# Kernel optimization log

Hardware: AMD Instinct MI355X
Metric: run time of the kernel (lower is better)

## Reference

```python
import jax, jax.numpy as jnp
import numpy as np

T = 0.1          # temperature from CLloss.__init__
PD_EPS = 1e-6    # nn.PairwiseDistance default eps (added to the difference)
NORM_EPS = 1e-12 # F.normalize eps


def setup_inputs() -> dict:
    key = jax.random.key(0)
    k1, k2 = jax.random.split(key)
    embed = jax.random.normal(k1, (16384, 2048), dtype=jnp.float32)
    labels = jax.random.randint(k2, (16384, 20), 0, 2, dtype=jnp.int32)
    return {"embed": embed, "labels": labels}


def reference(embed, labels):
    lab = labels.astype(jnp.float32)
    n = embed.shape[0]
    # F.normalize(embed, dim=-1): x / max(||x||, eps)
    norm = jnp.maximum(jnp.linalg.norm(embed, axis=-1, keepdims=True), NORM_EPS)
    e = embed / norm
    # NOTE: original torch code has `return loss` inside the outer loop, so only
    # anchor i=0 contributes. Faithfully reproduce that.
    # pairwise distance: ||e0 - ej + eps||_2 for j = 1..n-1
    d = jnp.linalg.norm(e[0] - e[1:] + PD_EPS, axis=-1)            # [n-1]
    log_sim = -d / T                                               # log exp(-d/t)
    c = jnp.dot(lab[1:], lab[0])                                   # [n-1] label overlap counts
    Ci = 1e-12 + jnp.sum(c)
    Ei = 1e-12 + jnp.sum(jnp.exp(log_sim))
    # Li = sum_j -(c_j/Ci) * log(exp(-d_j/t)/Ei)
    Li = jnp.sum(-(c / Ci) * (log_sim - jnp.log(Ei)))
    return Li / n
```

## Files before the change

kernel.cpp:

```cpp
#include <hip/hip_runtime.h>
#include <math.h>

#define NROW 16384
#define DIM 2048
#define NLAB 20
#define T_INV 10.0f
#define PD_EPS 1e-6f
#define NORM_EPS 1e-12f

#define MAIN_BLOCKS 1024
#define THREADS 256
#define WS_PARTIALS_OFS 2560

__global__ __launch_bounds__(THREADS) void prep_kernel(const float* __restrict__ embed,
                                                       float* __restrict__ ws) {
    __shared__ float red[THREADS / 64];
    const int tid = threadIdx.x;
    const int lane = tid & 63, wid = tid >> 6;

    const float4* row0 = (const float4*)embed;
    float s = 0.f;
    for (int i = tid; i < DIM / 4; i += THREADS) {
        float4 v = row0[i];
        s += v.x * v.x + v.y * v.y + v.z * v.z + v.w * v.w;
    }
    for (int o = 32; o; o >>= 1) s += __shfl_xor(s, o, 64);
    if (lane == 0) red[wid] = s;
    __syncthreads();
    float tot = red[0] + red[1] + red[2] + red[3];
    float inv = 1.0f / fmaxf(sqrtf(tot), NORM_EPS);

    float saa = 0.f;
    float4* a4 = (float4*)ws;
    for (int i = tid; i < DIM / 4; i += THREADS) {
        float4 v = row0[i];
        float4 w;
        w.x = v.x * inv + PD_EPS;
        w.y = v.y * inv + PD_EPS;
        w.z = v.z * inv + PD_EPS;
        w.w = v.w * inv + PD_EPS;
        a4[i] = w;
        saa += w.x * w.x + w.y * w.y + w.z * w.z + w.w * w.w;
    }
    for (int o = 32; o; o >>= 1) saa += __shfl_xor(saa, o, 64);
    __syncthreads();
    if (lane == 0) red[wid] = saa;
    __syncthreads();
    if (tid == 0) ws[DIM] = red[0] + red[1] + red[2] + red[3];
}

__global__ __launch_bounds__(THREADS) void main_kernel(const float* __restrict__ embed,
                                                       const int* __restrict__ labels,
                                                       const float* __restrict__ ws) {
    __shared__ float a_lds[DIM];
    __shared__ float wsum[THREADS / 64][3];

    const int tid = threadIdx.x;
    const int lane = tid & 63, wid = tid >> 6;

    {
        const float4* src = (const float4*)ws;
        float4* dst = (float4*)a_lds;
        for (int i = tid; i < DIM / 4; i += THREADS) dst[i] = src[i];
    }
    const float S_aa = ws[DIM];
    __syncthreads();

    const float lab0 = (lane < NLAB) ? (float)labels[lane] : 0.f;

    const int gw = blockIdx.x * (THREADS / 64) + wid;
    const int nwaves = gridDim.x * (THREADS / 64);

    float acc_e = 0.f, acc_c = 0.f, acc_cl = 0.f;

    for (int row = 1 + gw; row < NROW; row += nwaves) {
        const float4* b4 = (const float4*)(embed + (size_t)row * DIM);
        const float4* a4 = (const float4*)a_lds;
        float sab = 0.f, sbb = 0.f;
#pragma unroll
        for (int it = 0; it < DIM / 4 / 64; ++it) {
            float4 bv = b4[it * 64 + lane];
            float4 av = a4[it * 64 + lane];
            sab += av.x * bv.x + av.y * bv.y + av.z * bv.z + av.w * bv.w;
            sbb += bv.x * bv.x + bv.y * bv.y + bv.z * bv.z + bv.w * bv.w;
        }
        float c = (lane < NLAB) ? lab0 * (float)labels[row * NLAB + lane] : 0.f;

        for (int o = 32; o; o >>= 1) {
            sab += __shfl_xor(sab, o, 64);
            sbb += __shfl_xor(sbb, o, 64);
            c   += __shfl_xor(c,   o, 64);
        }
        float inv = 1.0f / fmaxf(sqrtf(sbb), NORM_EPS);
        float d2 = S_aa + inv * (inv * sbb - 2.0f * sab);
        d2 = fmaxf(d2, 0.f);
        float ls = -sqrtf(d2) * T_INV;
        acc_e += expf(ls);
        acc_c += c;
        acc_cl += c * ls;
    }

    if (lane == 0) {
        wsum[wid][0] = acc_e;
        wsum[wid][1] = acc_c;
        wsum[wid][2] = acc_cl;
    }
    __syncthreads();
    if (tid == 0) {
        float se = 0.f, sc = 0.f, scl = 0.f;
        for (int w = 0; w < THREADS / 64; ++w) {
            se += wsum[w][0];
            sc += wsum[w][1];
            scl += wsum[w][2];
        }
        float* p = (float*)wsum;
        (void)p;
        float* partials = (float*)0;
        (void)partials;
        ((float*)ws)[0] = ((float*)ws)[0];
        float* wsw = const_cast<float*>(ws);
        wsw[WS_PARTIALS_OFS + blockIdx.x * 3 + 0] = se;
        wsw[WS_PARTIALS_OFS + blockIdx.x * 3 + 1] = sc;
        wsw[WS_PARTIALS_OFS + blockIdx.x * 3 + 2] = scl;
    }
}

__global__ __launch_bounds__(THREADS) void final_kernel(const float* __restrict__ ws,
                                                        float* __restrict__ out) {
    __shared__ float red[THREADS / 64][3];
    const int tid = threadIdx.x;
    const int lane = tid & 63, wid = tid >> 6;

    float se = 0.f, sc = 0.f, scl = 0.f;
    for (int i = tid; i < MAIN_BLOCKS; i += THREADS) {
        se  += ws[WS_PARTIALS_OFS + i * 3 + 0];
        sc  += ws[WS_PARTIALS_OFS + i * 3 + 1];
        scl += ws[WS_PARTIALS_OFS + i * 3 + 2];
    }
    for (int o = 32; o; o >>= 1) {
        se  += __shfl_xor(se,  o, 64);
        sc  += __shfl_xor(sc,  o, 64);
        scl += __shfl_xor(scl, o, 64);
    }
    if (lane == 0) { red[wid][0] = se; red[wid][1] = sc; red[wid][2] = scl; }
    __syncthreads();
    if (tid == 0) {
        se = sc = scl = 0.f;
        for (int w = 0; w < THREADS / 64; ++w) {
            se += red[w][0]; sc += red[w][1]; scl += red[w][2];
        }
        float Ci = 1e-12f + sc;
        float Ei = 1e-12f + se;
        float Li = (sc * logf(Ei) - scl) / Ci;
        out[0] = Li / (float)NROW;
    }
}

extern "C" void kernel_launch(void* const* d_in, const int* in_sizes, int n_in,
                              void* d_out, int out_size, void* d_ws, size_t ws_size,
                              hipStream_t stream) {
    const float* embed = (const float*)d_in[0];
    const int* labels = (const int*)d_in[1];
    float* out = (float*)d_out;
    float* ws = (float*)d_ws;

    prep_kernel<<<1, THREADS, 0, stream>>>(embed, ws);
    main_kernel<<<MAIN_BLOCKS, THREADS, 0, stream>>>(embed, labels, ws);
    final_kernel<<<1, THREADS, 0, stream>>>(ws, out);
}
```

Before: 196.5 us.

## Fuse prep, main and final kernels into one kernel with atomic last-block reduction

Merges the three kernels into one. Each wave recomputes the normalized anchor row 0 into registers instead of staging it through workspace and LDS. Cross-block reduction now uses float atomics plus a completion counter, with the last block computing the loss. The grid doubles to 2048 blocks. This removes two launches and the serialized single-block prep and final phases, at the cost of a redundant row-0 read per wave, more registers, a memset, and nondeterministic float summation order.

```diff
diff --git a/kernel.cpp b/kernel.cpp
--- a/kernel.cpp
+++ b/kernel.cpp
@@ -8,81 +8,60 @@
 #define PD_EPS 1e-6f
 #define NORM_EPS 1e-12f
 
-#define MAIN_BLOCKS 1024
+#define BLOCKS 2048
 #define THREADS 256
-#define WS_PARTIALS_OFS 2560
+#define WPB (THREADS / 64)
+#define TOTAL_WAVES (BLOCKS * WPB)
+#define FRAG 8
 
-__global__ __launch_bounds__(THREADS) void prep_kernel(const float* __restrict__ embed,
-                                                       float* __restrict__ ws) {
-    __shared__ float red[THREADS / 64];
+
+__global__ __launch_bounds__(THREADS) void clloss_kernel(const float* __restrict__ embed,
+                                                         const int* __restrict__ labels,
+                                                         float* __restrict__ ws,
+                                                         float* __restrict__ out) {
     const int tid = threadIdx.x;
-    const int lane = tid & 63, wid = tid >> 6;
+    const int lane = tid & 63;
+    const int wid = tid >> 6;
 
     const float4* row0 = (const float4*)embed;
+    float4 v[FRAG];
+#pragma unroll
+    for (int it = 0; it < FRAG; ++it) v[it] = row0[it * 64 + lane];
+
     float s = 0.f;
-    for (int i = tid; i < DIM / 4; i += THREADS) {
-        float4 v = row0[i];
-        s += v.x * v.x + v.y * v.y + v.z * v.z + v.w * v.w;
-    }
+#pragma unroll
+    for (int it = 0; it < FRAG; ++it)
+        s += v[it].x * v[it].x + v[it].y * v[it].y + v[it].z * v[it].z + v[it].w * v[it].w;
     for (int o = 32; o; o >>= 1) s += __shfl_xor(s, o, 64);
-    if (lane == 0) red[wid] = s;
-    __syncthreads();
-    float tot = red[0] + red[1] + red[2] + red[3];
-    float inv = 1.0f / fmaxf(sqrtf(tot), NORM_EPS);
+    const float inv0 = 1.0f / fmaxf(sqrtf(s), NORM_EPS);
 
+    float4 av[FRAG];
     float saa = 0.f;
-    float4* a4 = (float4*)ws;
-    for (int i = tid; i < DIM / 4; i += THREADS) {
-        float4 v = row0[i];
-        float4 w;
-        w.x = v.x * inv + PD_EPS;
-        w.y = v.y * inv + PD_EPS;
-        w.z = v.z * inv + PD_EPS;
-        w.w = v.w * inv + PD_EPS;
-        a4[i] = w;
-        saa += w.x * w.x + w.y * w.y + w.z * w.z + w.w * w.w;
+#pragma unroll
+    for (int it = 0; it < FRAG; ++it) {
+        av[it].x = v[it].x * inv0 + PD_EPS;
+        av[it].y = v[it].y * inv0 + PD_EPS;
+        av[it].z = v[it].z * inv0 + PD_EPS;
+        av[it].w = v[it].w * inv0 + PD_EPS;
+        saa += av[it].x * av[it].x + av[it].y * av[it].y +
+               av[it].z * av[it].z + av[it].w * av[it].w;
     }
     for (int o = 32; o; o >>= 1) saa += __shfl_xor(saa, o, 64);
-    __syncthreads();
-    if (lane == 0) red[wid] = saa;
-    __syncthreads();
-    if (tid == 0) ws[DIM] = red[0] + red[1] + red[2] + red[3];
-}
-
-__global__ __launch_bounds__(THREADS) void main_kernel(const float* __restrict__ embed,
-                                                       const int* __restrict__ labels,
-                                                       const float* __restrict__ ws) {
-    __shared__ float a_lds[DIM];
-    __shared__ float wsum[THREADS / 64][3];
-
-    const int tid = threadIdx.x;
-    const int lane = tid & 63, wid = tid >> 6;
-
-    {
-        const float4* src = (const float4*)ws;
-        float4* dst = (float4*)a_lds;
-        for (int i = tid; i < DIM / 4; i += THREADS) dst[i] = src[i];
-    }
-    const float S_aa = ws[DIM];
-    __syncthreads();
+    const float S_aa = saa;
 
     const float lab0 = (lane < NLAB) ? (float)labels[lane] : 0.f;
 
-    const int gw = blockIdx.x * (THREADS / 64) + wid;
-    const int nwaves = gridDim.x * (THREADS / 64);
-
+    const int gw = blockIdx.x * WPB + wid;
     float acc_e = 0.f, acc_c = 0.f, acc_cl = 0.f;
 
-    for (int row = 1 + gw; row < NROW; row += nwaves) {
+    for (int row = 1 + gw; row < NROW; row += TOTAL_WAVES) {
         const float4* b4 = (const float4*)(embed + (size_t)row * DIM);
-        const float4* a4 = (const float4*)a_lds;
         float sab = 0.f, sbb = 0.f;
 #pragma unroll
-        for (int it = 0; it < DIM / 4 / 64; ++it) {
-            float4 bv = b4[it * 64 + lane];
-            float4 av = a4[it * 64 + lane];
-            sab += av.x * bv.x + av.y * bv.y + av.z * bv.z + av.w * bv.w;
-            sbb += bv.x * bv.x + bv.y * bv.y + bv.z * bv.z + bv.w * bv.w;
+        for (int it = 0; it < FRAG; ++it) {
+            float4 b = b4[it * 64 + lane];
+            sab += av[it].x * b.x + av[it].y * b.y + av[it].z * b.z + av[it].w * b.w;
+            sbb += b.x * b.x + b.y * b.y + b.z * b.z + b.w * b.w;
         }
         float c = (lane < NLAB) ? lab0 * (float)labels[row * NLAB + lane] : 0.f;
 
@@ -91,15 +70,15 @@
             sbb += __shfl_xor(sbb, o, 64);
             c   += __shfl_xor(c,   o, 64);
         }
-        float inv = 1.0f / fmaxf(sqrtf(sbb), NORM_EPS);
-        float d2 = S_aa + inv * (inv * sbb - 2.0f * sab);
-        d2 = fmaxf(d2, 0.f);
+        float invb = 1.0f / fmaxf(sqrtf(sbb), NORM_EPS);
+        float d2 = fmaxf(S_aa + invb * (invb * sbb - 2.0f * sab), 0.f);
         float ls = -sqrtf(d2) * T_INV;
-        acc_e += expf(ls);
-        acc_c += c;
+        acc_e  += expf(ls);
+        acc_c  += c;
         acc_cl += c * ls;
     }
 
+    __shared__ float wsum[WPB][3];
     if (lane == 0) {
         wsum[wid][0] = acc_e;
         wsum[wid][1] = acc_c;
@@ -108,51 +87,23 @@
     __syncthreads();
     if (tid == 0) {
         float se = 0.f, sc = 0.f, scl = 0.f;
-        for (int w = 0; w < THREADS / 64; ++w) {
-            se += wsum[w][0];
-            sc += wsum[w][1];
-            scl += wsum[w][2];
+        for (int w = 0; w < WPB; ++w) {
+            se += wsum[w][0]; sc += wsum[w][1]; scl += wsum[w][2];
         }
-        float* p = (float*)wsum;
-        (void)p;
-        float* partials = (float*)0;
-        (void)partials;
-        ((float*)ws)[0] = ((float*)ws)[0];
-        float* wsw = const_cast<float*>(ws);
-        wsw[WS_PARTIALS_OFS + blockIdx.x * 3 + 0] = se;
-        wsw[WS_PARTIALS_OFS + blockIdx.x * 3 + 1] = sc;
-        wsw[WS_PARTIALS_OFS + blockIdx.x * 3 + 2] = scl;
-    }
-}
-
-__global__ __launch_bounds__(THREADS) void final_kernel(const float* __restrict__ ws,
-                                                        float* __restrict__ out) {
-    __shared__ float red[THREADS / 64][3];
-    const int tid = threadIdx.x;
-    const int lane = tid & 63, wid = tid >> 6;
-
-    float se = 0.f, sc = 0.f, scl = 0.f;
-    for (int i = tid; i < MAIN_BLOCKS; i += THREADS) {
-        se  += ws[WS_PARTIALS_OFS + i * 3 + 0];
-        sc  += ws[WS_PARTIALS_OFS + i * 3 + 1];
-        scl += ws[WS_PARTIALS_OFS + i * 3 + 2];
-    }
-    for (int o = 32; o; o >>= 1) {
-        se  += __shfl_xor(se,  o, 64);
-        sc  += __shfl_xor(sc,  o, 64);
-        scl += __shfl_xor(scl, o, 64);
-    }
-    if (lane == 0) { red[wid][0] = se; red[wid][1] = sc; red[wid][2] = scl; }
-    __syncthreads();
-    if (tid == 0) {
-        se = sc = scl = 0.f;
-        for (int w = 0; w < THREADS / 64; ++w) {
-            se += red[w][0]; sc += red[w][1]; scl += red[w][2];
+        atomicAdd(&ws[0], se);
+        atomicAdd(&ws[1], sc);
+        atomicAdd(&ws[2], scl);
+        __threadfence();
+        unsigned prev = atomicAdd((unsigned*)&ws[3], 1u);
+        if (prev == (unsigned)(BLOCKS - 1)) {
+            float Se  = atomicAdd(&ws[0], 0.f);
+            float Sc  = atomicAdd(&ws[1], 0.f);
+            float Scl = atomicAdd(&ws[2], 0.f);
+            float Ci = 1e-12f + Sc;
+            float Ei = 1e-12f + Se;
+            float Li = (Sc * logf(Ei) - Scl) / Ci;
+            out[0] = Li / (float)NROW;
         }
-        float Ci = 1e-12f + sc;
-        float Ei = 1e-12f + se;
-        float Li = (sc * logf(Ei) - scl) / Ci;
-        out[0] = Li / (float)NROW;
     }
 }
 
@@ -164,7 +115,6 @@
     float* out = (float*)d_out;
     float* ws = (float*)d_ws;
 
-    prep_kernel<<<1, THREADS, 0, stream>>>(embed, ws);
-    main_kernel<<<MAIN_BLOCKS, THREADS, 0, stream>>>(embed, labels, ws);
-    final_kernel<<<1, THREADS, 0, stream>>>(ws, out);
+    hipMemsetAsync(ws, 0, 16, stream);
+    clloss_kernel<<<BLOCKS, THREADS, 0, stream>>>(embed, labels, ws, out);
 }
```

New measurement: 288.0 us. 46.6% more time.
